# Performance work log

Hardware: AMD Instinct MI355X
Metric: run time of the kernel (lower is better)

Reference implementation:

```python
import jax, jax.numpy as jnp
import numpy as np

B, N, L, H, D, IN = 512, 128, 10, 16, 8, 16
NT = B * N
E = NT * 16

def _lin(key, fan_in, shape):
    b = 1.0 / np.sqrt(fan_in)
    return jax.random.uniform(key, shape, jnp.float32, -b, b)

def setup_inputs() -> dict:
    key = jax.random.key(0)
    ks = jax.random.split(key, 12)
    x = jax.random.normal(ks[0], (NT, IN), jnp.float32)
    # within-graph random edges so to_dense_adj is well defined
    g = jax.random.randint(ks[1], (E,), 0, B)
    i = jax.random.randint(ks[2], (E,), 0, N)
    j = jax.random.randint(ks[3], (E,), 0, N)
    edge_index = jnp.stack([g * N + i, g * N + j]).astype(jnp.int32)
    return dict(
        x=x,
        gin_w1=_lin(ks[4], H, (2, L, H, H)),   # [ld/ud, layer, H, H]
        gin_b1=_lin(ks[5], H, (2, L, H)),
        gin_w2=_lin(ks[6], H, (2, L, H, H)),
        gin_b2=_lin(ks[7], H, (2, L, H)),
        mean_w=_lin(ks[8], H, (2, H, D)),
        mean_b=jnp.zeros((2, D), jnp.float32),
        std_w=_lin(ks[9], H, (2, H, D)),
        std_b=jnp.zeros((2, D), jnp.float32),
        edge_index=edge_index,
    )

def _encoder(x, w1, b1, w2, b2, mw, mb, sw, sb, src, dst):
    # PyG GIN stack: GINConv(MLP[Lin->ReLU->Lin]), eps=0, sum aggregation,
    # ReLU between layers (dropout = identity in eval mode).
    h = x
    for l in range(L):
        agg = jax.ops.segment_sum(h[src], dst, num_segments=NT)
        t = h + agg  # (1+eps)*x + sum_{j in N(i)} x_j with eps=0
        t = jnp.maximum(t @ w1[l] + b1[l], 0.0) @ w2[l] + b2[l]
        h = jnp.maximum(t, 0.0) if l < L - 1 else t
    mean = h @ mw + mb
    std = jax.nn.softplus(h @ sw + sb)
    return mean, std

def reference(x, gin_w1, gin_b1, gin_w2, gin_b2, mean_w, mean_b, std_w, std_b, edge_index):
    src, dst = edge_index[0], edge_index[1]
    enc = jax.vmap(_encoder, in_axes=(None, 0, 0, 0, 0, 0, 0, 0, 0, None, None))
    mean, std = enc(x, gin_w1, gin_b1, gin_w2, gin_b2,
                    mean_w, mean_b, std_w, std_b, src, dst)  # [2, NT, D]
    # reparameterized sample: eps ~ N(0,1) (prior.sample, detached)
    eps = jax.random.normal(jax.random.key(42), (2, NT, D), jnp.float32)
    z = mean + std * eps
    z_ld = z[0].reshape(B, N, D)
    z_ud = z[1].reshape(B, N, D)
    logits = jnp.einsum('bnd,bmd->bnm', z_ld, z_ud)  # per-graph inner-product decode
    dense_adj = jnp.zeros((B, N, N), jnp.float32).at[src // N, src % N, dst % N].add(1.0)
    n_pos = dense_adj.sum()
    posw = (B * N * N - n_pos) / n_pos
    # BCE-with-logits, pos_weight, reduction='sum'
    nll = jnp.sum(posw * dense_adj * jax.nn.softplus(-logits)
                  + (1.0 - dense_adj) * jax.nn.softplus(logits))
    # KL(N(mean,std) || N(0,1)), summed over both encoders
    kl = jnp.sum(-jnp.log(std) + 0.5 * (std * std + mean * mean) - 0.5)
    return nll, kl, jax.nn.sigmoid(logits), dense_adj
```

## Files before the change

kernel.cpp:

```cpp
#include <hip/hip_runtime.h>

#define B_    512
#define N_    128
#define L_    10
#define H_    16
#define D_    8
#define NT_   65536
#define E_    1048576
#define NNB_  8388608
#define CAP_  4096
#define CCAP_ 2816
#define HS_   20
#define PLANE_ (129*HS_ + 4)

__device__ __forceinline__ unsigned rotl32(unsigned v, int r){ return (v<<r)|(v>>(32-r)); }

__device__ __forceinline__ void threefry2x32(unsigned c0, unsigned c1, unsigned &o0, unsigned &o1){
  const unsigned ks0 = 0u, ks1 = 42u, ks2 = 0u ^ 42u ^ 0x1BD11BDAu;
  unsigned x0 = c0 + ks0, x1 = c1 + ks1;
#define TFR(r) { x0 += x1; x1 = rotl32(x1, r); x1 ^= x0; }
  TFR(13) TFR(15) TFR(26) TFR(6)   x0 += ks1; x1 += ks2 + 1u;
  TFR(17) TFR(29) TFR(16) TFR(24)  x0 += ks2; x1 += ks0 + 2u;
  TFR(13) TFR(15) TFR(26) TFR(6)   x0 += ks0; x1 += ks1 + 3u;
  TFR(17) TFR(29) TFR(16) TFR(24)  x0 += ks1; x1 += ks2 + 4u;
  TFR(13) TFR(15) TFR(26) TFR(6)   x0 += ks2; x1 += ks0 + 5u;
#undef TFR
  o0 = x0; o1 = x1;
}

__device__ __forceinline__ float erfinv_f(float x){
  float w = -log1pf(-x*x);
  float p;
  if (w < 5.0f) {
    w -= 2.5f;
    p = 2.81022636e-08f;
    p = fmaf(p, w, 3.43273939e-07f);
    p = fmaf(p, w, -3.5233877e-06f);
    p = fmaf(p, w, -4.39150654e-06f);
    p = fmaf(p, w, 0.00021858087f);
    p = fmaf(p, w, -0.00125372503f);
    p = fmaf(p, w, -0.00417768164f);
    p = fmaf(p, w, 0.246640727f);
    p = fmaf(p, w, 1.50140941f);
  } else {
    w = sqrtf(w) - 3.0f;
    p = -0.000200214257f;
    p = fmaf(p, w, 0.000100950558f);
    p = fmaf(p, w, 0.00134934322f);
    p = fmaf(p, w, -0.00367342844f);
    p = fmaf(p, w, 0.00573950773f);
    p = fmaf(p, w, -0.0076224613f);
    p = fmaf(p, w, 0.00943887047f);
    p = fmaf(p, w, 1.00167406f);
    p = fmaf(p, w, 2.83297682f);
  }
  return p * x;
}

__device__ __forceinline__ float softplus_f(float x){
  return fmaxf(x, 0.0f) + log1pf(expf(-fabsf(x)));
}

__device__ __forceinline__ void blockReduceAdd(double v, double* target){
  __shared__ double red[16];
  int lane = threadIdx.x & 63;
  int w    = threadIdx.x >> 6;
  #pragma unroll
  for(int off = 32; off > 0; off >>= 1) v += __shfl_down(v, off);
  if(lane == 0) red[w] = v;
  __syncthreads();
  if(threadIdx.x == 0){
    double s = red[0];
    int nw = (blockDim.x + 63) >> 6;
    for(int k = 1; k < nw; k++) s += red[k];
    atomicAdd(target, s);
  }
}

__global__ __launch_bounds__(1024)
void k_bin(const int* __restrict__ ei, int* __restrict__ gcount,
           unsigned short* __restrict__ ebuf){
  __shared__ int skv[4096];
  __shared__ int cnt[512];
  __shared__ int gb[512];
  __shared__ int off[512];
  __shared__ int wtot[8];
  const int t = threadIdx.x;
  if(t < 512) cnt[t] = 0;
  __syncthreads();
  int kv[4];
  const int base = blockIdx.x * 4096;
  #pragma unroll
  for(int k = 0; k < 4; k++){
    int e = base + k*1024 + t;
    int s = ei[e];
    int d = ei[E_ + e];
    int g = d >> 7;
    kv[k] = (g << 14) | ((s & 127) << 7) | (d & 127);
    atomicAdd(&cnt[g], 1);
  }
  __syncthreads();
  int intra = 0;
  if(t < 512){
    int lane = t & 63;
    int myc = cnt[t];
    int s = myc;
    #pragma unroll
    for(int o = 1; o < 64; o <<= 1){
      int v = __shfl_up(s, o);
      if(lane >= o) s += v;
    }
    intra = s - myc;
    if(lane == 63) wtot[t >> 6] = s;
    gb[t] = myc ? atomicAdd(&gcount[t], myc) : 0;
  }
  __syncthreads();
  if(t < 8){
    int v = wtot[t];
    int s = v;
    #pragma unroll
    for(int o = 1; o < 8; o <<= 1){
      int u = __shfl_up(s, o);
      if(t >= o) s += u;
    }
    wtot[t] = s - v;
  }
  if(t < 512) cnt[t] = 0;
  __syncthreads();
  if(t < 512) off[t] = intra + wtot[t >> 6];
  __syncthreads();
  #pragma unroll
  for(int k = 0; k < 4; k++){
    int g = kv[k] >> 14;
    int pos = atomicAdd(&cnt[g], 1);
    skv[off[g] + pos] = kv[k];
  }
  __syncthreads();
  #pragma unroll
  for(int k = 0; k < 4; k++){
    int i = k*1024 + t;
    int v = skv[i];
    int g = v >> 14;
    int idx = gb[g] + (i - off[g]);
    if(idx < CAP_) ebuf[(size_t)g*CAP_ + idx] = (unsigned short)(v & 0x3FFF);
  }
}

__global__ __launch_bounds__(1024, 8)
void k_mega(const float* __restrict__ x, const unsigned short* __restrict__ ebuf,
            const int* __restrict__ gcount,
            const float* __restrict__ gw1, const float* __restrict__ gb1,
            const float* __restrict__ gw2, const float* __restrict__ gb2,
            const float* __restrict__ mw,  const float* __restrict__ mb,
            const float* __restrict__ sw,  const float* __restrict__ sb,
            float* __restrict__ z, double* acc){
  __shared__ __align__(16) float hh[2*PLANE_];
  __shared__ __align__(16) float agg_l[2*128*HS_];
  __shared__ __align__(16) float u_l[2*128*HS_];
  __shared__ __align__(16) unsigned short col_l[CCAP_];
  __shared__ int off_l[129];

  const int b = blockIdx.x, t = threadIdx.x;
  const int n  = t & 127;
  const int q  = __builtin_amdgcn_readfirstlane((t >> 7) & 3);
  const int e  = __builtin_amdgcn_readfirstlane(t >> 9);
  const int q4 = q * 4;

  int* cnt = (int*)hh;

  if(t < 128) cnt[t] = 0;
  {
    uint4 s128; s128.x = s128.y = s128.z = s128.w = 0x00800080u;
    uint4* c4 = (uint4*)col_l;
    if(t < CCAP_/8) c4[t] = s128;
  }
  __syncthreads();

  int ec = gcount[b]; if(ec > CAP_) ec = CAP_;
  const unsigned short* eb = ebuf + (size_t)b*CAP_;
  for(int i = t; i < ec; i += 1024) atomicAdd(&cnt[eb[i] & 127], 1);
  __syncthreads();

  if(t < 64){
    int lane = t;
    int a0 = (cnt[lane]      + 3) & ~3;
    int a1 = (cnt[64 + lane] + 3) & ~3;
    int s0 = a0, s1 = a1;
    #pragma unroll
    for(int o = 1; o < 64; o <<= 1){
      int v0 = __shfl_up(s0, o);
      int v1 = __shfl_up(s1, o);
      if(lane >= o){ s0 += v0; s1 += v1; }
    }
    int totA = __shfl(s0, 63);
    off_l[lane]      = s0 - a0;
    off_l[64 + lane] = totA + s1 - a1;
    if(lane == 63) off_l[128] = totA + s1;
    cnt[lane] = 0; cnt[64 + lane] = 0;
  }
  __syncthreads();

  for(int i = t; i < ec; i += 1024){
    int pk = eb[i];
    int d = pk & 127;
    int pos = atomicAdd(&cnt[d], 1);
    int idx = off_l[d] + pos;
    if(idx < CCAP_) col_l[idx] = (unsigned short)(pk >> 7);
  }
  __syncthreads();
  const int r0 = off_l[n], r1 = off_l[n + 1];

  if(t < 512){
    const float4* x4 = (const float4*)x + (size_t)b*512;
    float4 v = x4[t];
    int row = t >> 2, c = (t & 3)*4;
    *(float4*)&hh[row*HS_ + c]          = v;
    *(float4*)&hh[PLANE_ + row*HS_ + c] = v;
  }
  if(t < 16){ hh[128*HS_ + t] = 0.0f; hh[PLANE_ + 128*HS_ + t] = 0.0f; }
  __syncthreads();

  const float* hb   = hh    + e*PLANE_;
  float*       aggb = agg_l + e*(128*HS_);
  float*       ub   = u_l   + e*(128*HS_);
  const float* w1g = gw1 + e*(L_*256);
  const float* w2g = gw2 + e*(L_*256);
  const float* b1g = gb1 + e*(L_*16);
  const float* b2g = gb2 + e*(L_*16);

  for(int l = 0; l < L_; l++){
    float ag0, ag1, ag2, ag3;
    {
      float4 s = *(const float4*)&hb[n*HS_ + q4];
      ag0 = s.x; ag1 = s.y; ag2 = s.z; ag3 = s.w;
    }
    for(int r = r0; r < r1; r += 4){
      ushort4 c4 = *(const ushort4*)&col_l[r];
      float4 v0 = *(const float4*)&hb[c4.x*HS_ + q4];
      float4 v1 = *(const float4*)&hb[c4.y*HS_ + q4];
      float4 v2 = *(const float4*)&hb[c4.z*HS_ + q4];
      float4 v3 = *(const float4*)&hb[c4.w*HS_ + q4];
      ag0 += v0.x + v1.x + v2.x + v3.x;
      ag1 += v0.y + v1.y + v2.y + v3.y;
      ag2 += v0.z + v1.z + v2.z + v3.z;
      ag3 += v0.w + v1.w + v2.w + v3.w;
    }
    *(float4*)&aggb[n*HS_ + q4] = make_float4(ag0, ag1, ag2, ag3);
    __syncthreads();

    float av[16];
    {
      const float4* ap = (const float4*)&aggb[n*HS_];
      float4 a0 = ap[0], a1 = ap[1], a2 = ap[2], a3 = ap[3];
      av[0]=a0.x; av[1]=a0.y; av[2]=a0.z; av[3]=a0.w;
      av[4]=a1.x; av[5]=a1.y; av[6]=a1.z; av[7]=a1.w;
      av[8]=a2.x; av[9]=a2.y; av[10]=a2.z; av[11]=a2.w;
      av[12]=a3.x; av[13]=a3.y; av[14]=a3.z; av[15]=a3.w;
    }
    const float* w1c = w1g + l*256 + q4;
    float u0 = b1g[l*16 + q4 + 0];
    float u1 = b1g[l*16 + q4 + 1];
    float u2 = b1g[l*16 + q4 + 2];
    float u3 = b1g[l*16 + q4 + 3];
    #pragma unroll
    for(int k = 0; k < 16; k++){
      float a = av[k];
      const float* wr = w1c + k*16;
      u0 = fmaf(a, wr[0], u0);
      u1 = fmaf(a, wr[1], u1);
      u2 = fmaf(a, wr[2], u2);
      u3 = fmaf(a, wr[3], u3);
    }
    u0 = fmaxf(u0, 0.0f); u1 = fmaxf(u1, 0.0f);
    u2 = fmaxf(u2, 0.0f); u3 = fmaxf(u3, 0.0f);
    *(float4*)&ub[n*HS_ + q4] = make_float4(u0, u1, u2, u3);
    __syncthreads();

    float uv[16];
    {
      const float4* up = (const float4*)&ub[n*HS_];
      float4 a0 = up[0], a1 = up[1], a2 = up[2], a3 = up[3];
      uv[0]=a0.x; uv[1]=a0.y; uv[2]=a0.z; uv[3]=a0.w;
      uv[4]=a1.x; uv[5]=a1.y; uv[6]=a1.z; uv[7]=a1.w;
      uv[8]=a2.x; uv[9]=a2.y; uv[10]=a2.z; uv[11]=a2.w;
      uv[12]=a3.x; uv[13]=a3.y; uv[14]=a3.z; uv[15]=a3.w;
    }
    const float* w2c = w2g + l*256 + q4;
    float o0 = b2g[l*16 + q4 + 0];
    float o1 = b2g[l*16 + q4 + 1];
    float o2 = b2g[l*16 + q4 + 2];
    float o3 = b2g[l*16 + q4 + 3];
    #pragma unroll
    for(int k = 0; k < 16; k++){
      float a = uv[k];
      const float* wr = w2c + k*16;
      o0 = fmaf(a, wr[0], o0);
      o1 = fmaf(a, wr[1], o1);
      o2 = fmaf(a, wr[2], o2);
      o3 = fmaf(a, wr[3], o3);
    }
    if(l < L_ - 1){
      o0 = fmaxf(o0, 0.0f); o1 = fmaxf(o1, 0.0f);
      o2 = fmaxf(o2, 0.0f); o3 = fmaxf(o3, 0.0f);
    }
    *(float4*)&hh[e*PLANE_ + n*HS_ + q4] = make_float4(o0, o1, o2, o3);
    __syncthreads();
  }

  float hv[16];
  {
    const float4* hp = (const float4*)&hb[n*HS_];
    float4 a0 = hp[0], a1 = hp[1], a2 = hp[2], a3 = hp[3];
    hv[0]=a0.x; hv[1]=a0.y; hv[2]=a0.z; hv[3]=a0.w;
    hv[4]=a1.x; hv[5]=a1.y; hv[6]=a1.z; hv[7]=a1.w;
    hv[8]=a2.x; hv[9]=a2.y; hv[10]=a2.z; hv[11]=a2.w;
    hv[12]=a3.x; hv[13]=a3.y; hv[14]=a3.z; hv[15]=a3.w;
  }
  const float* mwg = mw + e*128; const float* mbg = mb + e*8;
  const float* swg = sw + e*128; const float* sbg = sb + e*8;
  double kll = 0.0;
  float zv[2];
  unsigned nodeBase = ((unsigned)e*NT_ + (unsigned)(b*128 + n))*8u;
  #pragma unroll
  for(int dd = 0; dd < 2; dd++){
    int d = q*2 + dd;
    float mm = mbg[d], ss = sbg[d];
    #pragma unroll
    for(int k = 0; k < 16; k++){
      mm = fmaf(hv[k], mwg[k*8 + d], mm);
      ss = fmaf(hv[k], swg[k*8 + d], ss);
    }
    float stdv = softplus_f(ss);
    unsigned o0, o1; threefry2x32(0u, nodeBase + (unsigned)d, o0, o1);
    unsigned bits = o0 ^ o1;
    float uu = __uint_as_float((bits >> 9) | 0x3f800000u) - 1.0f;
    const float lo = -0.99999994f;
    float uval = fmaxf(lo, fmaf(uu, 2.0f, lo));
    float eps = 1.41421356f * erfinv_f(uval);
    zv[dd] = mm + stdv * eps;
    float stdc = fmaxf(stdv, 1e-37f);
    float term = 0.5f*(stdv*stdv + mm*mm) - logf(stdc) - 0.5f;
    if(!(term == term) || term > 1e30f) term = 1e30f;
    kll += (double)term;
  }
  *(float2*)&z[nodeBase + (unsigned)(q*2)] = make_float2(zv[0], zv[1]);
  blockReduceAdd(kll, acc + 1);
}

#define TSB_ 132
#define ZUS_ 10
__global__ __launch_bounds__(256, 8)
void k_decode(const float* __restrict__ z, const unsigned short* __restrict__ ebuf,
              const int* __restrict__ gcount, float* __restrict__ sig,
              float* __restrict__ adj, double* acc){
  __shared__ float zl[256];
  __shared__ float zu[128*ZUS_];
  __shared__ unsigned tile32[32*TSB_/4];
  const int b = blockIdx.x, cy = blockIdx.y, t = threadIdx.x;
  const int row0 = cy * 32;
  const float* zld = z + (size_t)b*1024 + (size_t)row0*8;
  const float* zud = z + (size_t)NT_*8 + (size_t)b*1024;
  for(int k = t; k < 1024; k += 256) zu[(k >> 3)*ZUS_ + (k & 7)] = zud[k];
  zl[t] = zld[t];
  for(int k = t; k < 32*TSB_/4; k += 256) tile32[k] = 0u;
  __syncthreads();
  {
    int ec = gcount[b]; if(ec > CAP_) ec = CAP_;
    const unsigned short* eb = ebuf + (size_t)b*CAP_;
    for(int qq = t; qq < ec; qq += 256){
      int pk = eb[qq];
      int r = (pk >> 7) - row0;
      if((unsigned)r < 32u){
        int cell = r*TSB_ + (pk & 127);
        atomicAdd(&tile32[cell >> 2], 1u << ((cell & 3)*8));
      }
    }
  }
  __syncthreads();
  const int c  = t & 127;
  const int rh = t >> 7;
  float zb[8];
  #pragma unroll
  for(int d = 0; d < 8; d++) zb[d] = zu[c*ZUS_ + d];
  float* sigb = sig + (size_t)b*16384 + (size_t)row0*128;
  float* adjb = adj + (size_t)b*16384 + (size_t)row0*128;
  const int sh = (c & 3)*8;
  float fl = 0.0f;
  #pragma unroll
  for(int rs = 0; rs < 16; rs++){
    int r = rh*16 + rs;
    const float* za = &zl[r*8];
    float xx = 0.0f;
    #pragma unroll
    for(int d = 0; d < 8; d++) xx = fmaf(za[d], zb[d], xx);
    unsigned packed = tile32[(r*TSB_ + c) >> 2];
    float ad = (float)((packed >> sh) & 0xFF);
    float sg = 1.0f / (1.0f + expf(-xx));
    float cc  = log1pf(expf(-fabsf(xx)));
    float spp = fmaxf(xx, 0.0f) + cc;
    float spn = fmaxf(-xx, 0.0f) + cc;
    fl += 7.0f*ad*spn + (1.0f - ad)*spp;
    sigb[r*128 + c] = sg;
    adjb[r*128 + c] = ad;
  }
  blockReduceAdd((double)fl, acc + 0);
}

__device__ __forceinline__ float clamp_finite(double v){
  if(v != v) return 0.0f;
  if(v >  3.3e38) return  3.3e38f;
  if(v < -3.3e38) return -3.3e38f;
  return (float)v;
}
__global__ void k_final(const double* __restrict__ acc, float* __restrict__ out){
  if(threadIdx.x == 0){
    out[0] = clamp_finite(acc[0]);
    out[1] = clamp_finite(acc[1]);
  }
}

extern "C" void kernel_launch(void* const* d_in, const int* in_sizes, int n_in,
                              void* d_out, int out_size, void* d_ws, size_t ws_size,
                              hipStream_t stream){
  const float* x   = (const float*)d_in[0];
  const float* gw1 = (const float*)d_in[1];
  const float* gb1 = (const float*)d_in[2];
  const float* gw2 = (const float*)d_in[3];
  const float* gb2 = (const float*)d_in[4];
  const float* mw  = (const float*)d_in[5];
  const float* mb  = (const float*)d_in[6];
  const float* sw  = (const float*)d_in[7];
  const float* sb  = (const float*)d_in[8];
  const int*   ei  = (const int*)d_in[9];

  float* out = (float*)d_out;
  float* sig = out + 2;
  float* adj = out + 2 + NNB_;

  char* ws = (char*)d_ws;
  int*            gcount = (int*)(ws);
  double*         acc    = (double*)(ws + 2048);
  unsigned short* ebuf   = (unsigned short*)(ws + 4096);
  float*          z      = (float*)(ws + 4096 + 2*512*CAP_);

  hipMemsetAsync(ws, 0, 4096, stream);

  k_bin   <<<E_/4096, 1024, 0, stream>>>(ei, gcount, ebuf);
  k_mega  <<<B_, 1024, 0, stream>>>(x, ebuf, gcount, gw1, gb1, gw2, gb2,
                                    mw, mb, sw, sb, z, acc);
  k_decode<<<dim3(B_, 4), 256, 0, stream>>>(z, ebuf, gcount, sig, adj, acc);
  k_final <<<1, 64, 0, stream>>>(acc, out);
}
```

Measured before the change: 219.4 us.

## Degree-sort nodes for gather balance, fuse final reduction, spread accumulators

In the GIN encoder kernel, nodes are bucket-sorted by in-degree and threads are remapped through a permutation. Threads in the same wavefront then walk neighbor lists of similar length, which reduces divergence in the gather loop. The decode kernel now processes a whole graph per 1024-thread block instead of four 256-thread blocks. The final scalar kernel is replaced by a last-block ticket reduction, and the double accumulators are spread across 16 padded slots to reduce atomic contention. The costs are extra shared-memory scans before the layer loop and lower decode occupancy from larger blocks.

```diff
diff --git a/kernel.cpp b/kernel.cpp
--- a/kernel.cpp
+++ b/kernel.cpp
@@ -77,6 +77,13 @@
   }
 }
 
+__device__ __forceinline__ float clamp_finite(double v){
+  if(v != v) return 0.0f;
+  if(v >  3.3e38) return  3.3e38f;
+  if(v < -3.3e38) return -3.3e38f;
+  return (float)v;
+}
+
 __global__ __launch_bounds__(1024)
 void k_bin(const int* __restrict__ ei, int* __restrict__ gcount,
            unsigned short* __restrict__ ebuf){
@@ -153,12 +160,14 @@
             const float* __restrict__ gw2, const float* __restrict__ gb2,
             const float* __restrict__ mw,  const float* __restrict__ mb,
             const float* __restrict__ sw,  const float* __restrict__ sb,
-            float* __restrict__ z, double* acc){
+            float* __restrict__ z, double* accb){
   __shared__ __align__(16) float hh[2*PLANE_];
   __shared__ __align__(16) float agg_l[2*128*HS_];
   __shared__ __align__(16) float u_l[2*128*HS_];
   __shared__ __align__(16) unsigned short col_l[CCAP_];
   __shared__ int off_l[129];
+  __shared__ int bkt_l[128];
+  __shared__ unsigned char perm_l[128];
 
   const int b = blockIdx.x, t = threadIdx.x;
   const int n  = t & 127;
@@ -207,9 +216,34 @@
     int idx = off_l[d] + pos;
     if(idx < CCAP_) col_l[idx] = (unsigned short)(pk >> 7);
   }
-  __syncthreads();
-  const int r0 = off_l[n], r1 = off_l[n + 1];
-
+  if(t < 128) bkt_l[t] = 0;
+  __syncthreads();
+
+  int key = 0;
+  if(t < 128){
+    key = (cnt[t] + 3) >> 2;
+    if(key > 127) key = 127;
+    atomicAdd(&bkt_l[key], 1);
+  }
+  __syncthreads();
+  if(t < 64){
+    int a0 = bkt_l[t], a1 = bkt_l[64 + t];
+    int s0 = a0, s1 = a1;
+    #pragma unroll
+    for(int o = 1; o < 64; o <<= 1){
+      int v0 = __shfl_up(s0, o);
+      int v1 = __shfl_up(s1, o);
+      if(t >= o){ s0 += v0; s1 += v1; }
+    }
+    int totA = __shfl(s0, 63);
+    bkt_l[t]      = s0 - a0;
+    bkt_l[64 + t] = totA + s1 - a1;
+  }
+  __syncthreads();
+  if(t < 128){
+    int pos = atomicAdd(&bkt_l[key], 1);
+    perm_l[pos] = (unsigned char)t;
+  }
   if(t < 512){
     const float4* x4 = (const float4*)x + (size_t)b*512;
     float4 v = x4[t];
@@ -219,6 +253,9 @@
   }
   if(t < 16){ hh[128*HS_ + t] = 0.0f; hh[PLANE_ + 128*HS_ + t] = 0.0f; }
   __syncthreads();
+
+  const int m   = perm_l[n];
+  const int mr0 = off_l[m], mr1 = off_l[m + 1];
 
   const float* hb   = hh    + e*PLANE_;
   float*       aggb = agg_l + e*(128*HS_);
@@ -231,10 +268,10 @@
   for(int l = 0; l < L_; l++){
     float ag0, ag1, ag2, ag3;
     {
-      float4 s = *(const float4*)&hb[n*HS_ + q4];
+      float4 s = *(const float4*)&hb[m*HS_ + q4];
       ag0 = s.x; ag1 = s.y; ag2 = s.z; ag3 = s.w;
     }
-    for(int r = r0; r < r1; r += 4){
+    for(int r = mr0; r < mr1; r += 4){
       ushort4 c4 = *(const ushort4*)&col_l[r];
       float4 v0 = *(const float4*)&hb[c4.x*HS_ + q4];
       float4 v1 = *(const float4*)&hb[c4.y*HS_ + q4];
@@ -245,7 +282,7 @@
       ag2 += v0.z + v1.z + v2.z + v3.z;
       ag3 += v0.w + v1.w + v2.w + v3.w;
     }
-    *(float4*)&aggb[n*HS_ + q4] = make_float4(ag0, ag1, ag2, ag3);
+    *(float4*)&aggb[m*HS_ + q4] = make_float4(ag0, ag1, ag2, ag3);
     __syncthreads();
 
     float av[16];
@@ -344,51 +381,48 @@
     kll += (double)term;
   }
   *(float2*)&z[nodeBase + (unsigned)(q*2)] = make_float2(zv[0], zv[1]);
-  blockReduceAdd(kll, acc + 1);
+  blockReduceAdd(kll, accb + 128 + (b & 15)*8);
 }
 
 #define TSB_ 132
 #define ZUS_ 10
-__global__ __launch_bounds__(256, 8)
+__global__ __launch_bounds__(1024, 2)
 void k_decode(const float* __restrict__ z, const unsigned short* __restrict__ ebuf,
               const int* __restrict__ gcount, float* __restrict__ sig,
-              float* __restrict__ adj, double* acc){
-  __shared__ float zl[256];
+              float* __restrict__ adj, double* accb, unsigned* ticket,
+              float* __restrict__ out){
+  __shared__ float zl[1024];
   __shared__ float zu[128*ZUS_];
-  __shared__ unsigned tile32[32*TSB_/4];
-  const int b = blockIdx.x, cy = blockIdx.y, t = threadIdx.x;
-  const int row0 = cy * 32;
-  const float* zld = z + (size_t)b*1024 + (size_t)row0*8;
+  __shared__ unsigned tile32[128*TSB_/4];
+  const int b = blockIdx.x, t = threadIdx.x;
+  const float* zld = z + (size_t)b*1024;
   const float* zud = z + (size_t)NT_*8 + (size_t)b*1024;
-  for(int k = t; k < 1024; k += 256) zu[(k >> 3)*ZUS_ + (k & 7)] = zud[k];
   zl[t] = zld[t];
-  for(int k = t; k < 32*TSB_/4; k += 256) tile32[k] = 0u;
+  zu[(t >> 3)*ZUS_ + (t & 7)] = zud[t];
+  for(int k = t; k < 128*TSB_/4; k += 1024) tile32[k] = 0u;
   __syncthreads();
   {
     int ec = gcount[b]; if(ec > CAP_) ec = CAP_;
     const unsigned short* eb = ebuf + (size_t)b*CAP_;
-    for(int qq = t; qq < ec; qq += 256){
+    for(int qq = t; qq < ec; qq += 1024){
       int pk = eb[qq];
-      int r = (pk >> 7) - row0;
-      if((unsigned)r < 32u){
-        int cell = r*TSB_ + (pk & 127);
-        atomicAdd(&tile32[cell >> 2], 1u << ((cell & 3)*8));
-      }
+      int cell = (pk >> 7)*TSB_ + (pk & 127);
+      atomicAdd(&tile32[cell >> 2], 1u << ((cell & 3)*8));
     }
   }
   __syncthreads();
   const int c  = t & 127;
-  const int rh = t >> 7;
+  const int rq = t >> 7;
   float zb[8];
   #pragma unroll
   for(int d = 0; d < 8; d++) zb[d] = zu[c*ZUS_ + d];
-  float* sigb = sig + (size_t)b*16384 + (size_t)row0*128;
-  float* adjb = adj + (size_t)b*16384 + (size_t)row0*128;
+  float* sigb = sig + (size_t)b*16384;
+  float* adjb = adj + (size_t)b*16384;
   const int sh = (c & 3)*8;
   float fl = 0.0f;
   #pragma unroll
   for(int rs = 0; rs < 16; rs++){
-    int r = rh*16 + rs;
+    int r = rq*16 + rs;
     const float* za = &zl[r*8];
     float xx = 0.0f;
     #pragma unroll
@@ -403,19 +437,21 @@
     sigb[r*128 + c] = sg;
     adjb[r*128 + c] = ad;
   }
-  blockReduceAdd((double)fl, acc + 0);
-}
-
-__device__ __forceinline__ float clamp_finite(double v){
-  if(v != v) return 0.0f;
-  if(v >  3.3e38) return  3.3e38f;
-  if(v < -3.3e38) return -3.3e38f;
-  return (float)v;
-}
-__global__ void k_final(const double* __restrict__ acc, float* __restrict__ out){
-  if(threadIdx.x == 0){
-    out[0] = clamp_finite(acc[0]);
-    out[1] = clamp_finite(acc[1]);
+  blockReduceAdd((double)fl, accb + (b & 15)*8);
+
+  if(t == 0){
+    __threadfence();
+    unsigned prev = atomicAdd(ticket, 1u);
+    if(prev == (unsigned)(B_ - 1)){
+      double nl = 0.0, kl = 0.0;
+      #pragma unroll
+      for(int i = 0; i < 16; i++){
+        nl += atomicAdd(&accb[i*8], 0.0);
+        kl += atomicAdd(&accb[128 + i*8], 0.0);
+      }
+      out[0] = clamp_finite(nl);
+      out[1] = clamp_finite(kl);
+    }
   }
 }
 
@@ -439,15 +475,15 @@
 
   char* ws = (char*)d_ws;
   int*            gcount = (int*)(ws);
-  double*         acc    = (double*)(ws + 2048);
-  unsigned short* ebuf   = (unsigned short*)(ws + 4096);
-  float*          z      = (float*)(ws + 4096 + 2*512*CAP_);
-
-  hipMemsetAsync(ws, 0, 4096, stream);
+  double*         accb   = (double*)(ws + 2048);
+  unsigned*       ticket = (unsigned*)(ws + 4096);
+  unsigned short* ebuf   = (unsigned short*)(ws + 8192);
+  float*          z      = (float*)(ws + 8192 + 2*512*CAP_);
+
+  hipMemsetAsync(ws, 0, 8192, stream);
 
   k_bin   <<<E_/4096, 1024, 0, stream>>>(ei, gcount, ebuf);
   k_mega  <<<B_, 1024, 0, stream>>>(x, ebuf, gcount, gw1, gb1, gw2, gb2,
-                                    mw, mb, sw, sb, z, acc);
-  k_decode<<<dim3(B_, 4), 256, 0, stream>>>(z, ebuf, gcount, sig, adj, acc);
-  k_final <<<1, 64, 0, stream>>>(acc, out);
-}
+                                    mw, mb, sw, sb, z, accb);
+  k_decode<<<B_, 1024, 0, stream>>>(z, ebuf, gcount, sig, adj, accb, ticket, out);
+}
```

New measurement: 240.4 us. +9.5%, slower.
